# Kernel tuning notes

Hardware: AMD Instinct MI355X
Metric: run time of the kernel (lower is better)

The kernel has to match this reference:

```python
import jax, jax.numpy as jnp
import numpy as np

LM_TEMP = 2.0      # opts.lm_temp
LAMBDA_SH = 20.0   # lambda_sh passed in ot_loss
EPS = 1e-8


def sinkhorn(M, a, b, lam, num_iter_max=1000, stop_thr=0.005):
    """Faithful port of sinkhorn_pytorch. M:[S,V], a:[S,B], b:[V,B]."""
    K = jnp.exp(-M * lam)          # [S,V]
    KM = K * M
    u0 = jnp.ones_like(a) / a.shape[0]
    v0 = jnp.zeros_like(b)

    def cond(state):
        cpt, u, v, err = state
        return (cpt < num_iter_max) & (err > stop_thr)

    def body(state):
        cpt, u, v, err = state
        u = a / (K @ (b / (u.T @ K).T))   # fused fixed-point step
        cpt = cpt + 1
        do_check = ((cpt % 20) == 1) | (cpt == num_iter_max)

        def check(uve):
            u, v, _ = uve
            v = b / (K.T @ u)
            u = a / (K @ v)
            bb = v * (K.T @ u)
            err = jnp.max(jnp.sum(jnp.abs(bb - b), axis=0))  # inf-norm over batch
            return u, v, err

        u, v, err = jax.lax.cond(do_check, check, lambda t: t, (u, v, err))
        return cpt, u, v, err

    state0 = (jnp.asarray(0, jnp.int32), u0, v0, jnp.asarray(1.0, M.dtype))
    _, u, v, _ = jax.lax.while_loop(cond, body, state0)
    return jnp.sum(u * (KM @ v), axis=0)   # [B] sinkhorn divergences


def setup_inputs() -> dict:
    key = jax.random.key(0)
    ks = jax.random.split(key, 6)
    B, H, V, NV, MAX_SLOTS = 512, 1024, 28996, 3000, 33
    inputs = jax.random.normal(ks[0], (B, 2 * H), jnp.float32)
    outputs = jax.random.normal(ks[1], (B, 512), jnp.float32)
    W_lm = jax.random.normal(ks[2], (V, H), jnp.float32) * 0.02   # lm head (no bias)
    W_lin = jax.random.normal(ks[3], (MAX_SLOTS, 512), jnp.float32) * 0.05
    b_lin = jnp.zeros((MAX_SLOTS,), jnp.float32)
    topics = jax.random.normal(ks[4], (MAX_SLOTS - 1, H), jnp.float32) * 0.01
    verbs = jax.random.randint(ks[5], (NV,), 0, V)
    return {"inputs": inputs, "outputs": outputs, "W_lm": W_lm,
            "W_lin": W_lin, "b_lin": b_lin, "topics": topics,
            "verbs": verbs, "nslots": 33}


def reference(inputs, outputs, W_lm, W_lin, b_lin, topics, verbs, nslots):
    H = W_lm.shape[1]
    # gather verb rows of the lm head once: logits[:, verbs] == x @ W_lm[verbs].T
    W_v = W_lm[verbs]                               # [NV, H]
    Wt = W_v.T                                      # [H, NV]
    o11 = jax.nn.softmax((inputs[:, :H] @ Wt) / LM_TEMP, axis=-1)
    o12 = jax.nn.softmax((inputs[:, H:] @ Wt) / LM_TEMP, axis=-1)
    o1 = (o11 + o12) * 0.5
    o1 = o1 / jnp.sum(o1, axis=1, keepdims=True)    # [B, NV] vocab marginals
    o2 = jax.nn.softmax((outputs @ W_lin.T + b_lin)[:, 1:nslots], axis=-1)  # [B, S]
    # cosine-distance cost matrix between topics and verb embeddings
    tn = topics[:nslots - 1]
    tn = tn / (jnp.linalg.norm(tn, axis=1, keepdims=True) + EPS)
    vn = W_v / (jnp.linalg.norm(W_v, axis=1, keepdims=True) + EPS)
    M = 1.0 - tn @ vn.T                             # [S, NV]
    # single chunk of ot_loss (B <= 1024): mean sinkhorn divergence
    return jnp.mean(sinkhorn(M, o2.T, o1.T, LAMBDA_SH))
```

## Files before the change

kernel.cpp:

```cpp
#include <hip/hip_runtime.h>

#define NV 3000
#define HH 1024
#define BB 512

typedef __attribute__((ext_vector_type(8))) short short8;
typedef __attribute__((ext_vector_type(4))) float floatx4;

__device__ __forceinline__ float wave_sum(float x) {
#pragma unroll
  for (int off = 32; off; off >>= 1) x += __shfl_xor(x, off, 64);
  return x;
}
__device__ __forceinline__ unsigned bf16r(float x) {
  unsigned u = __float_as_uint(x);
  u += 0x7fffu + ((u >> 16) & 1u);
  return u >> 16;
}
__device__ __forceinline__ void gload16(const void* g, void* l) {
  __builtin_amdgcn_global_load_lds(
      (const __attribute__((address_space(1))) unsigned*)g,
      (__attribute__((address_space(3))) unsigned*)l, 16, 0, 0);
}

__global__ __launch_bounds__(256) void norms_wb_kernel(
    const float* __restrict__ W_lm, const float* __restrict__ topics,
    const int* __restrict__ verbs, float* __restrict__ vninv,
    float* __restrict__ tninv, unsigned short* __restrict__ Wb) {
  int r = blockIdx.x, t = threadIdx.x;
  bool isW = r < 3072;
  int j = isW ? (r < NV ? r : NV - 1) : 0;
  const float* src = isW ? (W_lm + (size_t)verbs[j] * HH)
                         : (topics + (size_t)(r - 3072) * HH);
  float4 v = *(const float4*)(src + t * 4);
  if (isW) {
    *(uint2*)(Wb + (size_t)r * HH + t * 4) =
        make_uint2(bf16r(v.x) | (bf16r(v.y) << 16),
                   bf16r(v.z) | (bf16r(v.w) << 16));
  }
  float ss = v.x * v.x + v.y * v.y + v.z * v.z + v.w * v.w;
  ss = wave_sum(ss);
  __shared__ float sq[4];
  if ((t & 63) == 0) sq[t >> 6] = ss;
  __syncthreads();
  if (t == 0) {
    float inv = 1.0f / (sqrtf(sq[0] + sq[1] + sq[2] + sq[3]) + 1e-8f);
    if (isW) { if (r < NV) vninv[r] = inv; }
    else tninv[r - 3072] = inv;
  }
}

__global__ __launch_bounds__(256) void xb_kernel(
    const float* __restrict__ inputs, unsigned short* __restrict__ Xb) {
  int idx = blockIdx.x * 256 + threadIdx.x;
  int r = idx >> 7, c8 = (idx & 127) << 3;
  const float* src = (r < 512) ? (inputs + (size_t)r * 2048 + c8)
                               : (inputs + (size_t)(r - 512) * 2048 + 1024 + c8);
  float4 x0 = ((const float4*)src)[0];
  float4 x1 = ((const float4*)src)[1];
  uint4 o;
  o.x = bf16r(x0.x) | (bf16r(x0.y) << 16);
  o.y = bf16r(x0.z) | (bf16r(x0.w) << 16);
  o.z = bf16r(x1.x) | (bf16r(x1.y) << 16);
  o.w = bf16r(x1.z) | (bf16r(x1.w) << 16);
  *(uint4*)(Xb + (size_t)r * HH + c8) = o;
}

__global__ __launch_bounds__(256) void topt_kernel(
    const float* __restrict__ topics, const float* __restrict__ tninv,
    float* __restrict__ topT) {
  int idx = blockIdx.x * 256 + threadIdx.x;
  int k = idx >> 5, s = idx & 31;
  topT[idx] = topics[(size_t)s * HH + k] * tninv[s];
}

__global__ __launch_bounds__(64) void a_kernel(
    const float* __restrict__ outputs, const float* __restrict__ W_lin,
    const float* __restrict__ b_lin, float* __restrict__ aT) {
  int r = blockIdx.x, t = threadIdx.x;
  __shared__ float orow[512];
  __shared__ float lg[33];
  __shared__ float ms[2];
  *(float4*)(orow + t * 8)     = *(const float4*)(outputs + (size_t)r * 512 + t * 8);
  *(float4*)(orow + t * 8 + 4) = *(const float4*)(outputs + (size_t)r * 512 + t * 8 + 4);
  __syncthreads();
  if (t < 33) {
    float acc = b_lin[t];
    for (int k = 0; k < 512; ++k) acc = fmaf(orow[k], W_lin[(size_t)t * 512 + k], acc);
    lg[t] = acc;
  }
  __syncthreads();
  if (t == 0) {
    float m = lg[1];
    for (int i = 2; i < 33; ++i) m = fmaxf(m, lg[i]);
    float ssum = 0.0f;
    for (int i = 1; i < 33; ++i) ssum += __expf(lg[i] - m);
    ms[0] = m; ms[1] = ssum;
  }
  __syncthreads();
  if (t >= 1 && t < 33) aT[(size_t)r * 32 + t - 1] = __expf(lg[t] - ms[0]) / ms[1];
}

__global__ __launch_bounds__(256) void gemm_mfma(
    const unsigned short* __restrict__ Xb, const unsigned short* __restrict__ Wb,
    float* __restrict__ L) {
  __shared__ unsigned short As[128 * 32], Bs[128 * 32];
  int t = threadIdx.x;
  int wave = t >> 6, ln = t & 63;
  int bn = blockIdx.x, bm = blockIdx.y;
  int wm = (wave >> 1) * 64, wn = (wave & 1) * 64;
  const unsigned short* ga = Xb + (size_t)(bm * 128 + (t >> 2)) * HH + (t & 3) * 8;
  const unsigned short* gb = Wb + (size_t)(bn * 128 + (t >> 2)) * HH + (t & 3) * 8;
  int lq = ln >> 4, lm = ln & 15;
  floatx4 acc[4][4];
#pragma unroll
  for (int i = 0; i < 4; ++i)
#pragma unroll
    for (int j = 0; j < 4; ++j) acc[i][j] = (floatx4)0.0f;

  for (int k0 = 0; k0 < HH; k0 += 32) {
    __syncthreads();
    gload16(ga + k0, As + t * 8);
    gload16(ga + (size_t)64 * HH + k0, As + 2048 + t * 8);
    gload16(gb + k0, Bs + t * 8);
    gload16(gb + (size_t)64 * HH + k0, Bs + 2048 + t * 8);
    __syncthreads();
    short8 af[4], bfr[4];
#pragma unroll
    for (int i = 0; i < 4; ++i)
      af[i] = *(const short8*)(As + (wm + i * 16 + lm) * 32 + lq * 8);
#pragma unroll
    for (int j = 0; j < 4; ++j)
      bfr[j] = *(const short8*)(Bs + (wn + j * 16 + lm) * 32 + lq * 8);
#pragma unroll
    for (int i = 0; i < 4; ++i)
#pragma unroll
      for (int j = 0; j < 4; ++j)
        acc[i][j] = __builtin_amdgcn_mfma_f32_16x16x32_bf16(af[i], bfr[j], acc[i][j], 0, 0, 0);
  }
  int row0 = bm * 128 + wm + lq * 4;
  int col0 = bn * 128 + wn + lm;
#pragma unroll
  for (int j = 0; j < 4; ++j) {
    int col = col0 + j * 16;
    if (col < NV) {
#pragma unroll
      for (int i = 0; i < 4; ++i) {
#pragma unroll
        for (int r = 0; r < 4; ++r)
          L[(size_t)(row0 + i * 16 + r) * NV + col] = acc[i][j][r] * 0.5f;
      }
    }
  }
}

__global__ __launch_bounds__(256) void softmax_kernel(
    float* __restrict__ L1, const float* __restrict__ L2) {
  int r = blockIdx.x, t = threadIdx.x, w = t >> 6, ln = t & 63;
  float* row1 = L1 + (size_t)r * NV;
  const float* row2 = L2 + (size_t)r * NV;
  __shared__ float rd[2][4];
  float s1 = 0.0f, s2 = 0.0f;
  for (int v = t; v < NV; v += 256) { s1 += __expf(row1[v]); s2 += __expf(row2[v]); }
  s1 = wave_sum(s1); s2 = wave_sum(s2);
  if (ln == 0) { rd[0][w] = s1; rd[1][w] = s2; }
  __syncthreads();
  s1 = rd[0][0] + rd[0][1] + rd[0][2] + rd[0][3];
  s2 = rd[1][0] + rd[1][1] + rd[1][2] + rd[1][3];
  float i1 = 0.5f / s1, i2 = 0.5f / s2;
  float rs = 0.0f;
  for (int v = t; v < NV; v += 256) {
    float o = __expf(row1[v]) * i1 + __expf(row2[v]) * i2;
    row1[v] = o; rs += o;
  }
  rs = wave_sum(rs);
  __syncthreads();
  if (ln == 0) rd[0][w] = rs;
  __syncthreads();
  float rinv = 1.0f / (rd[0][0] + rd[0][1] + rd[0][2] + rd[0][3]);
  for (int v = t; v < NV; v += 256) row1[v] *= rinv;
}

__global__ __launch_bounds__(256) void mk_kernel(
    const float* __restrict__ W_lm, const int* __restrict__ verbs,
    const float* __restrict__ topT, const float* __restrict__ vninv,
    unsigned* __restrict__ Kb, float* __restrict__ KMt) {
  __shared__ float red[4][64][33];
  int t = threadIdx.x, ln = t & 63, w = t >> 6;
  int v = blockIdx.x * 64 + ln;
  int vc = v < NV ? v : NV - 1;
  int kb = __builtin_amdgcn_readfirstlane(w) << 8;
  const float* wrow = W_lm + (size_t)verbs[vc] * HH + kb;
  const float* tb = topT + (size_t)kb * 32;
  float acc[32];
#pragma unroll
  for (int s = 0; s < 32; ++s) acc[s] = 0.0f;
  for (int kk = 0; kk < 256; kk += 4) {
    float4 w4 = *(const float4*)(wrow + kk);
    const float* tr = tb + kk * 32;
    const float* pw = (const float*)&w4;
#pragma unroll
    for (int d = 0; d < 4; ++d)
#pragma unroll
      for (int s = 0; s < 32; ++s) acc[s] = fmaf(pw[d], tr[d * 32 + s], acc[s]);
  }
#pragma unroll
  for (int s = 0; s < 32; ++s) red[w][ln][s] = acc[s];
  __syncthreads();
  for (int idx = t; idx < 1024; idx += 256) {
    int l = idx >> 4, pr = idx & 15;
    int vo = blockIdx.x * 64 + l;
    if (vo < NV) {
      int s0 = pr * 2, s1 = s0 + 1;
      float vi = vninv[vo];
      float d0 = red[0][l][s0] + red[1][l][s0] + red[2][l][s0] + red[3][l][s0];
      float d1 = red[0][l][s1] + red[1][l][s1] + red[2][l][s1] + red[3][l][s1];
      float M0 = 1.0f - d0 * vi, M1 = 1.0f - d1 * vi;
      float K0 = __expf(-20.0f * M0), K1 = __expf(-20.0f * M1);
      *(float2*)(KMt + (size_t)vo * 32 + s0) = make_float2(K0 * M0, K1 * M1);
      Kb[(size_t)vo * 16 + pr] = bf16r(K0) | (bf16r(K1) << 16);
    }
  }
}

__device__ __forceinline__ void gridbar(unsigned* bar, unsigned target) {
  __syncthreads();
  if (threadIdx.x == 0) {
    __hip_atomic_fetch_add(bar, 1u, __ATOMIC_RELEASE, __HIP_MEMORY_SCOPE_AGENT);
    while (__hip_atomic_load(bar, __ATOMIC_ACQUIRE, __HIP_MEMORY_SCOPE_AGENT) < target) {
      __builtin_amdgcn_s_sleep(1);
    }
  }
  __syncthreads();
}

#define UNPK(q, o)                                          \
  kc[(o) + 0] = __uint_as_float((q).x << 16);               \
  kc[(o) + 1] = __uint_as_float((q).x & 0xffff0000u);       \
  kc[(o) + 2] = __uint_as_float((q).y << 16);               \
  kc[(o) + 3] = __uint_as_float((q).y & 0xffff0000u);       \
  kc[(o) + 4] = __uint_as_float((q).z << 16);               \
  kc[(o) + 5] = __uint_as_float((q).z & 0xffff0000u);       \
  kc[(o) + 6] = __uint_as_float((q).w << 16);               \
  kc[(o) + 7] = __uint_as_float((q).w & 0xffff0000u);

template <bool STORE_T>
__device__ __forceinline__ void kpass_ss(
    const uint4* __restrict__ Kb, const float* __restrict__ bsh0,
    const float* __restrict__ bsh1, const float* u0, const float* u1,
    float* z0, float* z1, float* vsh0, float* vsh1, int pid, int p) {
#pragma unroll 3
  for (int i = 0; i < 6; ++i) {
    int v = pid + (i << 9);
    if (i < 5 || v < NV) {
      const uint4* kq = Kb + ((size_t)v << 2) + (p << 1);
      uint4 q0 = kq[0], q1 = kq[1];
      float kc[16];
      UNPK(q0, 0) UNPK(q1, 8)
      float w0 = 0.0f, w1 = 0.0f;
#pragma unroll
      for (int s = 0; s < 16; ++s) { w0 = fmaf(kc[s], u0[s], w0); w1 = fmaf(kc[s], u1[s], w1); }
      w0 += __shfl_xor(w0, 1, 64);
      w1 += __shfl_xor(w1, 1, 64);
      float t0 = bsh0[v] * __builtin_amdgcn_rcpf(w0);
      float t1 = bsh1[v] * __builtin_amdgcn_rcpf(w1);
      if (STORE_T && !p) { vsh0[v] = t0; vsh1[v] = t1; }
#pragma unroll
      for (int s = 0; s < 16; ++s) { z0[s] = fmaf(kc[s], t0, z0[s]); z1[s] = fmaf(kc[s], t1, z1[s]); }
    }
  }
}

__device__ __forceinline__ void errpass_ss(
    const uint4* __restrict__ Kb, const float* __restrict__ bsh0,
    const float* __restrict__ bsh1, const float* u0, const float* u1,
    const float* vsh0, const float* vsh1, float& ep0, float& ep1,
    int pid, int p) {
#pragma unroll 3
  for (int i = 0; i < 6; ++i) {
    int v = pid + (i << 9);
    if (i < 5 || v < NV) {
      const uint4* kq = Kb + ((size_t)v << 2) + (p << 1);
      uint4 q0 = kq[0], q1 = kq[1];
      float kc[16];
      UNPK(q0, 0) UNPK(q1, 8)
      float w0 = 0.0f, w1 = 0.0f;
#pragma unroll
      for (int s = 0; s < 16; ++s) { w0 = fmaf(kc[s], u0[s], w0); w1 = fmaf(kc[s], u1[s], w1); }
      w0 += __shfl_xor(w0, 1, 64);
      w1 += __shfl_xor(w1, 1, 64);
      if (!p) {
        ep0 += fabsf(vsh0[v] * w0 - bsh0[v]);
        ep1 += fabsf(vsh1[v] * w1 - bsh1[v]);
      }
    }
  }
}

__device__ __forceinline__ float waveRS16(float* z, int ln) {
  int cnt = 16;
#pragma unroll
  for (int d = 2; d <= 16; d <<= 1) {
    int half = cnt >> 1;
    bool hi = (ln & d) != 0;
#pragma unroll
    for (int k = 0; k < 8; ++k) {
      if (k < half) {
        float a = z[k], b = z[half + k];
        z[k] = hi ? b : a;
        z[half + k] = hi ? a : b;
      }
    }
#pragma unroll
    for (int k = 0; k < 8; ++k)
      if (k < half) z[k] += __shfl_xor(z[half + k], d, 64);
    cnt = half;
  }
  return z[0] + __shfl_xor(z[0], 32, 64);
}

__global__ __launch_bounds__(1024) void sinkhorn_kernel(
    const uint4* __restrict__ Kb, const float* __restrict__ KMt,
    const float* __restrict__ bT, const float* __restrict__ aT,
    unsigned* __restrict__ slots, float* __restrict__ outp) {
  const int t = threadIdx.x;
  const int w = t >> 6, ln = t & 63;
  const int p = t & 1, pid = t >> 1;
  const int col0 = blockIdx.x << 1;
  const float* b0r = bT + (size_t)col0 * NV;
  const float* b1r = b0r + NV;
  float* accres = (float*)(slots + 64);
  unsigned* bar = slots + 65;

  __shared__ float zred[2][16][32];
  __shared__ float ush[2][32];
  __shared__ float sredA[16], sredB[16];
  __shared__ unsigned ebits;
  __shared__ float vsh0[3072], vsh1[3072];
  __shared__ float bsh0[3072], bsh1[3072];
  float* ushf = &ush[0][0];

  const int sl = ((ln & 1) << 4) | ((ln & 2) << 2) | (ln & 4) |
                 ((ln & 8) >> 2) | ((ln & 16) >> 4);

  for (int idx = t; idx < NV; idx += 1024) { bsh0[idx] = b0r[idx]; bsh1[idx] = b1r[idx]; }
  float areg = (t < 64) ? aT[(size_t)col0 * 32 + t] : 0.0f;

  float u0[16], u1[16];
#pragma unroll
  for (int s = 0; s < 16; ++s) { u0[s] = 1.0f / 32.0f; u1[s] = 1.0f / 32.0f; }
  if (t < 64) ushf[t] = 1.0f / 32.0f;
  __syncthreads();
  float err = 1.0f;
  int cpt = 0, chk = 0;
  unsigned barcnt = 0;

  while (cpt < 1000 && err > 0.005f) {
    float z0[16], z1[16];
#pragma unroll
    for (int s = 0; s < 16; ++s) { z0[s] = 0.0f; z1[s] = 0.0f; }
    kpass_ss<false>(Kb, bsh0, bsh1, u0, u1, z0, z1, vsh0, vsh1, pid, p);
    float r0 = waveRS16(z0, ln), r1 = waveRS16(z1, ln);
    __syncthreads();
    if (ln < 32) { zred[0][w][sl] = r0; zred[1][w][sl] = r1; }
    __syncthreads();
    if (t < 64) {
      int c = t >> 5, s = t & 31;
      float zz = 0.0f;
#pragma unroll
      for (int k = 0; k < 16; ++k) zz += zred[c][k][s];
      ushf[t] = areg * __builtin_amdgcn_rcpf(zz);
    }
    __syncthreads();
#pragma unroll
    for (int q = 0; q < 4; ++q) {
      *(float4*)(u0 + q * 4) = *(float4*)(&ush[0][(p << 4) + q * 4]);
      *(float4*)(u1 + q * 4) = *(float4*)(&ush[1][(p << 4) + q * 4]);
    }
    ++cpt;

    if (cpt % 20 == 1 || cpt == 1000) {
#pragma unroll
      for (int s = 0; s < 16; ++s) { z0[s] = 0.0f; z1[s] = 0.0f; }
      kpass_ss<true>(Kb, bsh0, bsh1, u0, u1, z0, z1, vsh0, vsh1, pid, p);
      r0 = waveRS16(z0, ln); r1 = waveRS16(z1, ln);
      __syncthreads();
      if (ln < 32) { zred[0][w][sl] = r0; zred[1][w][sl] = r1; }
      __syncthreads();
      if (t < 64) {
        int c = t >> 5, s = t & 31;
        float zz = 0.0f;
#pragma unroll
        for (int k = 0; k < 16; ++k) zz += zred[c][k][s];
        ushf[t] = areg * __builtin_amdgcn_rcpf(zz);
      }
      __syncthreads();
#pragma unroll
      for (int q = 0; q < 4; ++q) {
        *(float4*)(u0 + q * 4) = *(float4*)(&ush[0][(p << 4) + q * 4]);
        *(float4*)(u1 + q * 4) = *(float4*)(&ush[1][(p << 4) + q * 4]);
      }
      float ep0 = 0.0f, ep1 = 0.0f;
      errpass_ss(Kb, bsh0, bsh1, u0, u1, vsh0, vsh1, ep0, ep1, pid, p);
      ep0 = wave_sum(ep0); ep1 = wave_sum(ep1);
      if (ln == 0) { sredA[w] = ep0; sredB[w] = ep1; }
      __syncthreads();
      if (t == 0) {
        float e0 = 0.0f, e1 = 0.0f;
#pragma unroll
        for (int k = 0; k < 16; ++k) { e0 += sredA[k]; e1 += sredB[k]; }
        atomicMax(slots + chk, __float_as_uint(fmaxf(e0, e1)));
      }
      ++barcnt;
      gridbar(bar, barcnt * 256u);
      if (t == 0) ebits = __hip_atomic_load(slots + chk, __ATOMIC_RELAXED, __HIP_MEMORY_SCOPE_AGENT);
      __syncthreads();
      err = __uint_as_float(ebits);
      ++chk;
    }
  }

  float y0[16], y1[16];
#pragma unroll
  for (int s = 0; s < 16; ++s) { y0[s] = 0.0f; y1[s] = 0.0f; }
#pragma unroll 3
  for (int i = 0; i < 6; ++i) {
    int v = pid + (i << 9);
    if (i < 5 || v < NV) {
      const float4* kp = (const float4*)(KMt + (size_t)v * 32 + (p << 4));
      float kc[16];
#pragma unroll
      for (int q = 0; q < 4; ++q) *(float4*)(kc + q * 4) = kp[q];
      float x0 = vsh0[v], x1 = vsh1[v];
#pragma unroll
      for (int s = 0; s < 16; ++s) { y0[s] = fmaf(kc[s], x0, y0[s]); y1[s] = fmaf(kc[s], x1, y1[s]); }
    }
  }
  float r0 = waveRS16(y0, ln), r1 = waveRS16(y1, ln);
  __syncthreads();
  if (ln < 32) { zred[0][w][sl] = r0; zred[1][w][sl] = r1; }
  __syncthreads();
  if (t < 64) {
    int c = t >> 5, s = t & 31;
    float ys = 0.0f;
#pragma unroll
    for (int k = 0; k < 16; ++k) ys += zred[c][k][s];
    float pp = ys * ushf[t];
#pragma unroll
    for (int off = 1; off <= 16; off <<= 1) pp += __shfl_xor(pp, off, 64);
    float other = __shfl_xor(pp, 32, 64);
    if (t == 0) atomicAdd(accres, pp + other);
  }
  ++barcnt;
  gridbar(bar, barcnt * 256u);
  if (blockIdx.x == 0 && t == 0) {
    unsigned ab = __hip_atomic_load((unsigned*)accres, __ATOMIC_RELAXED, __HIP_MEMORY_SCOPE_AGENT);
    outp[0] = __uint_as_float(ab) / 512.0f;
  }
}

extern "C" void kernel_launch(void* const* d_in, const int* in_sizes, int n_in,
                              void* d_out, int out_size, void* d_ws, size_t ws_size,
                              hipStream_t stream) {
  (void)in_sizes; (void)n_in; (void)out_size; (void)ws_size;
  const float* inputs  = (const float*)d_in[0];
  const float* outputs = (const float*)d_in[1];
  const float* W_lm    = (const float*)d_in[2];
  const float* W_lin   = (const float*)d_in[3];
  const float* b_lin   = (const float*)d_in[4];
  const float* topics  = (const float*)d_in[5];
  const int*   verbs   = (const int*)d_in[6];
  float* out = (float*)d_out;

  char* ws = (char*)d_ws;
  float*    L     = (float*)(ws);
  float*    L1    = L;
  float*    L2    = (float*)(ws + 6144000);
  float*    aT    = (float*)(ws + 12288000);
  unsigned* Kb    = (unsigned*)(ws + 12353536);
  float*    KMt   = (float*)(ws + 12545536);
  float*    topT  = (float*)(ws + 12929536);
  float*    vninv = (float*)(ws + 13060608);
  float*    tninv = (float*)(ws + 13072640);
  unsigned* slots = (unsigned*)(ws + 13072768);
  unsigned short* Xb = (unsigned short*)(ws + 13073280);
  unsigned short* Wb = (unsigned short*)(ws + 15170432);

  hipMemsetAsync((void*)slots, 0, 512, stream);

  norms_wb_kernel<<<3104, 256, 0, stream>>>(W_lm, topics, verbs, vninv, tninv, Wb);
  xb_kernel<<<512, 256, 0, stream>>>(inputs, Xb);
  topt_kernel<<<128, 256, 0, stream>>>(topics, tninv, topT);
  a_kernel<<<BB, 64, 0, stream>>>(outputs, W_lin, b_lin, aT);
  gemm_mfma<<<dim3(24, 8), 256, 0, stream>>>(Xb, Wb, L);
  softmax_kernel<<<BB, 256, 0, stream>>>(L1, L2);
  mk_kernel<<<47, 256, 0, stream>>>(W_lm, verbs, topT, vninv, Kb, KMt);
  sinkhorn_kernel<<<256, 1024, 0, stream>>>((const uint4*)Kb, KMt, L1, aT, slots, out);
}
```

Measured before the change: 412.7 us.

## Store Sinkhorn kernel matrix in per-column scaled FP8 and fold error pass into next iteration

The Sinkhorn K matrix is now stored as FP8 with a per-verb scale factor (KM is multiplied by the same factor), halving the bytes read on every iteration. The separate error-check pass is removed: the residual is instead accumulated during the following regular iteration's K·u product, which removes one full pass over K per check. Smaller changes come along: softmax caches exponentials in LDS instead of recomputing them, the a_kernel dot product is vectorised, and the gload helper is inlined. FP8 quantisation of K risks accuracy loss, and deferring the error check by one iteration may change when the loop stops.

```diff
diff --git a/kernel.cpp b/kernel.cpp
--- a/kernel.cpp
+++ b/kernel.cpp
@@ -6,6 +6,7 @@
 
 typedef __attribute__((ext_vector_type(8))) short short8;
 typedef __attribute__((ext_vector_type(4))) float floatx4;
+typedef __attribute__((ext_vector_type(2))) float floatx2;
 
 __device__ __forceinline__ float wave_sum(float x) {
 #pragma unroll
@@ -17,10 +18,36 @@
   u += 0x7fffu + ((u >> 16) & 1u);
   return u >> 16;
 }
-__device__ __forceinline__ void gload16(const void* g, void* l) {
-  __builtin_amdgcn_global_load_lds(
-      (const __attribute__((address_space(1))) unsigned*)g,
-      (__attribute__((address_space(3))) unsigned*)l, 16, 0, 0);
+
+__device__ __forceinline__ unsigned pk4_fp8(float a, float b, float c, float d) {
+#if __has_builtin(__builtin_amdgcn_cvt_pk_fp8_f32)
+  int r = __builtin_amdgcn_cvt_pk_fp8_f32(a, b, 0, false);
+  r = __builtin_amdgcn_cvt_pk_fp8_f32(c, d, r, true);
+  return (unsigned)r;
+#else
+  float v4[4] = {a, b, c, d};
+  unsigned out = 0;
+#pragma unroll
+  for (int i = 0; i < 4; ++i) {
+    unsigned bb = __float_as_uint(v4[i]);
+    bb += 0x7ffffu + ((bb >> 20) & 1u);
+    int e8 = (int)(bb >> 23) - 120;
+    unsigned byte = (e8 <= 0) ? 0u : (((unsigned)e8 << 3) | ((bb >> 20) & 7u));
+    out |= byte << (8 * i);
+  }
+  return out;
+#endif
+}
+__device__ __forceinline__ void unpk4(unsigned q, float* kc) {
+#if __has_builtin(__builtin_amdgcn_cvt_pk_f32_fp8)
+  floatx2 lo = __builtin_amdgcn_cvt_pk_f32_fp8((int)q, false);
+  floatx2 hi = __builtin_amdgcn_cvt_pk_f32_fp8((int)q, true);
+  kc[0] = lo[0]; kc[1] = lo[1]; kc[2] = hi[0]; kc[3] = hi[1];
+#else
+#pragma unroll
+  for (int i = 0; i < 4; ++i)
+    kc[i] = __uint_as_float((((q >> (8 * i)) & 0x7fu) << 20) + 0x3C000000u) - 0.0078125f;
+#endif
 }
 
 __global__ __launch_bounds__(256) void norms_wb_kernel(
@@ -85,9 +112,14 @@
   *(float4*)(orow + t * 8 + 4) = *(const float4*)(outputs + (size_t)r * 512 + t * 8 + 4);
   __syncthreads();
   if (t < 33) {
-    float acc = b_lin[t];
-    for (int k = 0; k < 512; ++k) acc = fmaf(orow[k], W_lin[(size_t)t * 512 + k], acc);
-    lg[t] = acc;
+    float4 a4 = make_float4(0.f, 0.f, 0.f, 0.f);
+    for (int k = 0; k < 512; k += 4) {
+      float4 o = *(const float4*)(orow + k);
+      float4 wl = *(const float4*)(W_lin + (size_t)t * 512 + k);
+      a4.x = fmaf(o.x, wl.x, a4.x); a4.y = fmaf(o.y, wl.y, a4.y);
+      a4.z = fmaf(o.z, wl.z, a4.z); a4.w = fmaf(o.w, wl.w, a4.w);
+    }
+    lg[t] = a4.x + a4.y + a4.z + a4.w + b_lin[t];
   }
   __syncthreads();
   if (t == 0) {
@@ -120,10 +152,18 @@
 
   for (int k0 = 0; k0 < HH; k0 += 32) {
     __syncthreads();
-    gload16(ga + k0, As + t * 8);
-    gload16(ga + (size_t)64 * HH + k0, As + 2048 + t * 8);
-    gload16(gb + k0, Bs + t * 8);
-    gload16(gb + (size_t)64 * HH + k0, Bs + 2048 + t * 8);
+    __builtin_amdgcn_global_load_lds(
+        (const __attribute__((address_space(1))) unsigned*)(ga + k0),
+        (__attribute__((address_space(3))) unsigned*)(As + t * 8), 16, 0, 0);
+    __builtin_amdgcn_global_load_lds(
+        (const __attribute__((address_space(1))) unsigned*)(ga + (size_t)64 * HH + k0),
+        (__attribute__((address_space(3))) unsigned*)(As + 2048 + t * 8), 16, 0, 0);
+    __builtin_amdgcn_global_load_lds(
+        (const __attribute__((address_space(1))) unsigned*)(gb + k0),
+        (__attribute__((address_space(3))) unsigned*)(Bs + t * 8), 16, 0, 0);
+    __builtin_amdgcn_global_load_lds(
+        (const __attribute__((address_space(1))) unsigned*)(gb + (size_t)64 * HH + k0),
+        (__attribute__((address_space(3))) unsigned*)(Bs + 2048 + t * 8), 16, 0, 0);
     __syncthreads();
     short8 af[4], bfr[4];
 #pragma unroll
@@ -159,9 +199,13 @@
   int r = blockIdx.x, t = threadIdx.x, w = t >> 6, ln = t & 63;
   float* row1 = L1 + (size_t)r * NV;
   const float* row2 = L2 + (size_t)r * NV;
+  __shared__ float e1[NV], e2[NV];
   __shared__ float rd[2][4];
   float s1 = 0.0f, s2 = 0.0f;
-  for (int v = t; v < NV; v += 256) { s1 += __expf(row1[v]); s2 += __expf(row2[v]); }
+  for (int v = t; v < NV; v += 256) {
+    float a = __expf(row1[v]), b = __expf(row2[v]);
+    e1[v] = a; e2[v] = b; s1 += a; s2 += b;
+  }
   s1 = wave_sum(s1); s2 = wave_sum(s2);
   if (ln == 0) { rd[0][w] = s1; rd[1][w] = s2; }
   __syncthreads();
@@ -170,22 +214,23 @@
   float i1 = 0.5f / s1, i2 = 0.5f / s2;
   float rs = 0.0f;
   for (int v = t; v < NV; v += 256) {
-    float o = __expf(row1[v]) * i1 + __expf(row2[v]) * i2;
-    row1[v] = o; rs += o;
+    float o = e1[v] * i1 + e2[v] * i2;
+    e1[v] = o; rs += o;
   }
   rs = wave_sum(rs);
   __syncthreads();
   if (ln == 0) rd[0][w] = rs;
   __syncthreads();
   float rinv = 1.0f / (rd[0][0] + rd[0][1] + rd[0][2] + rd[0][3]);
-  for (int v = t; v < NV; v += 256) row1[v] *= rinv;
+  for (int v = t; v < NV; v += 256) row1[v] = e1[v] * rinv;
 }
 
 __global__ __launch_bounds__(256) void mk_kernel(
     const float* __restrict__ W_lm, const int* __restrict__ verbs,
     const float* __restrict__ topT, const float* __restrict__ vninv,
-    unsigned* __restrict__ Kb, float* __restrict__ KMt) {
+    unsigned* __restrict__ Kb8, float* __restrict__ KMt) {
   __shared__ float red[4][64][33];
+  __shared__ float kv[64][33], km[64][33];
   int t = threadIdx.x, ln = t & 63, w = t >> 6;
   int v = blockIdx.x * 64 + ln;
   int vc = v < NV ? v : NV - 1;
@@ -207,18 +252,32 @@
 #pragma unroll
   for (int s = 0; s < 32; ++s) red[w][ln][s] = acc[s];
   __syncthreads();
-  for (int idx = t; idx < 1024; idx += 256) {
-    int l = idx >> 4, pr = idx & 15;
+  for (int idx = t; idx < 2048; idx += 256) {
+    int l = idx >> 5, s = idx & 31;
     int vo = blockIdx.x * 64 + l;
+    float vi = vninv[vo < NV ? vo : NV - 1];
+    float d = red[0][l][s] + red[1][l][s] + red[2][l][s] + red[3][l][s];
+    float M = 1.0f - d * vi;
+    float K = __expf(-20.0f * M);
+    kv[l][s] = K; km[l][s] = K * M;
+  }
+  __syncthreads();
+  if (t < 64) {
+    int vo = blockIdx.x * 64 + t;
     if (vo < NV) {
-      int s0 = pr * 2, s1 = s0 + 1;
-      float vi = vninv[vo];
-      float d0 = red[0][l][s0] + red[1][l][s0] + red[2][l][s0] + red[3][l][s0];
-      float d1 = red[0][l][s1] + red[1][l][s1] + red[2][l][s1] + red[3][l][s1];
-      float M0 = 1.0f - d0 * vi, M1 = 1.0f - d1 * vi;
-      float K0 = __expf(-20.0f * M0), K1 = __expf(-20.0f * M1);
-      *(float2*)(KMt + (size_t)vo * 32 + s0) = make_float2(K0 * M0, K1 * M1);
-      Kb[(size_t)vo * 16 + pr] = bf16r(K0) | (bf16r(K1) << 16);
+      float mx = 0.0f;
+#pragma unroll
+      for (int s = 0; s < 32; ++s) mx = fmaxf(mx, kv[t][s]);
+      float c = 240.0f / mx;
+      unsigned pk[8];
+#pragma unroll
+      for (int q = 0; q < 8; ++q)
+        pk[q] = pk4_fp8(kv[t][4 * q] * c, kv[t][4 * q + 1] * c,
+                        kv[t][4 * q + 2] * c, kv[t][4 * q + 3] * c);
+      *(uint4*)(Kb8 + (size_t)vo * 8)     = make_uint4(pk[0], pk[1], pk[2], pk[3]);
+      *(uint4*)(Kb8 + (size_t)vo * 8 + 4) = make_uint4(pk[4], pk[5], pk[6], pk[7]);
+#pragma unroll
+      for (int s = 0; s < 32; ++s) KMt[(size_t)vo * 32 + s] = km[t][s] * c;
     }
   }
 }
@@ -234,65 +293,34 @@
   __syncthreads();
 }
 
-#define UNPK(q, o)                                          \
-  kc[(o) + 0] = __uint_as_float((q).x << 16);               \
-  kc[(o) + 1] = __uint_as_float((q).x & 0xffff0000u);       \
-  kc[(o) + 2] = __uint_as_float((q).y << 16);               \
-  kc[(o) + 3] = __uint_as_float((q).y & 0xffff0000u);       \
-  kc[(o) + 4] = __uint_as_float((q).z << 16);               \
-  kc[(o) + 5] = __uint_as_float((q).z & 0xffff0000u);       \
-  kc[(o) + 6] = __uint_as_float((q).w << 16);               \
-  kc[(o) + 7] = __uint_as_float((q).w & 0xffff0000u);
-
-template <bool STORE_T>
+template <bool STORE_T, bool MEASURE>
 __device__ __forceinline__ void kpass_ss(
-    const uint4* __restrict__ Kb, const float* __restrict__ bsh0,
+    const uint4* __restrict__ Kb8, const float* __restrict__ bsh0,
     const float* __restrict__ bsh1, const float* u0, const float* u1,
-    float* z0, float* z1, float* vsh0, float* vsh1, int pid, int p) {
+    float* z0, float* z1, float* vsh0, float* vsh1,
+    float& ep0, float& ep1, int pid, int p) {
 #pragma unroll 3
   for (int i = 0; i < 6; ++i) {
     int v = pid + (i << 9);
     if (i < 5 || v < NV) {
-      const uint4* kq = Kb + ((size_t)v << 2) + (p << 1);
-      uint4 q0 = kq[0], q1 = kq[1];
+      uint4 q = Kb8[(size_t)v * 2 + p];
       float kc[16];
-      UNPK(q0, 0) UNPK(q1, 8)
+      unpk4(q.x, kc); unpk4(q.y, kc + 4); unpk4(q.z, kc + 8); unpk4(q.w, kc + 12);
       float w0 = 0.0f, w1 = 0.0f;
 #pragma unroll
       for (int s = 0; s < 16; ++s) { w0 = fmaf(kc[s], u0[s], w0); w1 = fmaf(kc[s], u1[s], w1); }
       w0 += __shfl_xor(w0, 1, 64);
       w1 += __shfl_xor(w1, 1, 64);
-      float t0 = bsh0[v] * __builtin_amdgcn_rcpf(w0);
-      float t1 = bsh1[v] * __builtin_amdgcn_rcpf(w1);
+      float b0v = bsh0[v], b1v = bsh1[v];
+      if (MEASURE && !p) {
+        ep0 += fabsf(vsh0[v] * w0 - b0v);
+        ep1 += fabsf(vsh1[v] * w1 - b1v);
+      }
+      float t0 = b0v * __builtin_amdgcn_rcpf(w0);
+      float t1 = b1v * __builtin_amdgcn_rcpf(w1);
       if (STORE_T && !p) { vsh0[v] = t0; vsh1[v] = t1; }
 #pragma unroll
       for (int s = 0; s < 16; ++s) { z0[s] = fmaf(kc[s], t0, z0[s]); z1[s] = fmaf(kc[s], t1, z1[s]); }
-    }
-  }
-}
-
-__device__ __forceinline__ void errpass_ss(
-    const uint4* __restrict__ Kb, const float* __restrict__ bsh0,
-    const float* __restrict__ bsh1, const float* u0, const float* u1,
-    const float* vsh0, const float* vsh1, float& ep0, float& ep1,
-    int pid, int p) {
-#pragma unroll 3
-  for (int i = 0; i < 6; ++i) {
-    int v = pid + (i << 9);
-    if (i < 5 || v < NV) {
-      const uint4* kq = Kb + ((size_t)v << 2) + (p << 1);
-      uint4 q0 = kq[0], q1 = kq[1];
-      float kc[16];
-      UNPK(q0, 0) UNPK(q1, 8)
-      float w0 = 0.0f, w1 = 0.0f;
-#pragma unroll
-      for (int s = 0; s < 16; ++s) { w0 = fmaf(kc[s], u0[s], w0); w1 = fmaf(kc[s], u1[s], w1); }
-      w0 += __shfl_xor(w0, 1, 64);
-      w1 += __shfl_xor(w1, 1, 64);
-      if (!p) {
-        ep0 += fabsf(vsh0[v] * w0 - bsh0[v]);
-        ep1 += fabsf(vsh1[v] * w1 - bsh1[v]);
-      }
     }
   }
 }
@@ -320,7 +348,7 @@
 }
 
 __global__ __launch_bounds__(1024) void sinkhorn_kernel(
-    const uint4* __restrict__ Kb, const float* __restrict__ KMt,
+    const uint4* __restrict__ Kb8, const float* __restrict__ KMt,
     const float* __restrict__ bT, const float* __restrict__ aT,
     unsigned* __restrict__ slots, float* __restrict__ outp) {
   const int t = threadIdx.x;
@@ -351,15 +379,19 @@
   for (int s = 0; s < 16; ++s) { u0[s] = 1.0f / 32.0f; u1[s] = 1.0f / 32.0f; }
   if (t < 64) ushf[t] = 1.0f / 32.0f;
   __syncthreads();
-  float err = 1.0f;
+  float err = 1.0f, ep0 = 0.0f, ep1 = 0.0f;
   int cpt = 0, chk = 0;
   unsigned barcnt = 0;
+  bool measuring = false;
 
   while (cpt < 1000 && err > 0.005f) {
     float z0[16], z1[16];
 #pragma unroll
     for (int s = 0; s < 16; ++s) { z0[s] = 0.0f; z1[s] = 0.0f; }
-    kpass_ss<false>(Kb, bsh0, bsh1, u0, u1, z0, z1, vsh0, vsh1, pid, p);
+    if (measuring)
+      kpass_ss<false, true>(Kb8, bsh0, bsh1, u0, u1, z0, z1, vsh0, vsh1, ep0, ep1, pid, p);
+    else
+      kpass_ss<false, false>(Kb8, bsh0, bsh1, u0, u1, z0, z1, vsh0, vsh1, ep0, ep1, pid, p);
     float r0 = waveRS16(z0, ln), r1 = waveRS16(z1, ln);
     __syncthreads();
     if (ln < 32) { zred[0][w][sl] = r0; zred[1][w][sl] = r1; }
@@ -379,29 +411,7 @@
     }
     ++cpt;
 
-    if (cpt % 20 == 1 || cpt == 1000) {
-#pragma unroll
-      for (int s = 0; s < 16; ++s) { z0[s] = 0.0f; z1[s] = 0.0f; }
-      kpass_ss<true>(Kb, bsh0, bsh1, u0, u1, z0, z1, vsh0, vsh1, pid, p);
-      r0 = waveRS16(z0, ln); r1 = waveRS16(z1, ln);
-      __syncthreads();
-      if (ln < 32) { zred[0][w][sl] = r0; zred[1][w][sl] = r1; }
-      __syncthreads();
-      if (t < 64) {
-        int c = t >> 5, s = t & 31;
-        float zz = 0.0f;
-#pragma unroll
-        for (int k = 0; k < 16; ++k) zz += zred[c][k][s];
-        ushf[t] = areg * __builtin_amdgcn_rcpf(zz);
-      }
-      __syncthreads();
-#pragma unroll
-      for (int q = 0; q < 4; ++q) {
-        *(float4*)(u0 + q * 4) = *(float4*)(&ush[0][(p << 4) + q * 4]);
-        *(float4*)(u1 + q * 4) = *(float4*)(&ush[1][(p << 4) + q * 4]);
-      }
-      float ep0 = 0.0f, ep1 = 0.0f;
-      errpass_ss(Kb, bsh0, bsh1, u0, u1, vsh0, vsh1, ep0, ep1, pid, p);
+    if (measuring) {
       ep0 = wave_sum(ep0); ep1 = wave_sum(ep1);
       if (ln == 0) { sredA[w] = ep0; sredB[w] = ep1; }
       __syncthreads();
@@ -417,6 +427,32 @@
       __syncthreads();
       err = __uint_as_float(ebits);
       ++chk;
+      ep0 = 0.0f; ep1 = 0.0f;
+      measuring = false;
+    }
+
+    if (err > 0.005f && cpt % 20 == 1) {
+#pragma unroll
+      for (int s = 0; s < 16; ++s) { z0[s] = 0.0f; z1[s] = 0.0f; }
+      kpass_ss<true, false>(Kb8, bsh0, bsh1, u0, u1, z0, z1, vsh0, vsh1, ep0, ep1, pid, p);
+      r0 = waveRS16(z0, ln); r1 = waveRS16(z1, ln);
+      __syncthreads();
+      if (ln < 32) { zred[0][w][sl] = r0; zred[1][w][sl] = r1; }
+      __syncthreads();
+      if (t < 64) {
+        int c = t >> 5, s = t & 31;
+        float zz = 0.0f;
+#pragma unroll
+        for (int k = 0; k < 16; ++k) zz += zred[c][k][s];
+        ushf[t] = areg * __builtin_amdgcn_rcpf(zz);
+      }
+      __syncthreads();
+#pragma unroll
+      for (int q = 0; q < 4; ++q) {
+        *(float4*)(u0 + q * 4) = *(float4*)(&ush[0][(p << 4) + q * 4]);
+        *(float4*)(u1 + q * 4) = *(float4*)(&ush[1][(p << 4) + q * 4]);
+      }
+      measuring = true;
     }
   }
 
@@ -477,14 +513,14 @@
   float*    L1    = L;
   float*    L2    = (float*)(ws + 6144000);
   float*    aT    = (float*)(ws + 12288000);
-  unsigned* Kb    = (unsigned*)(ws + 12353536);
-  float*    KMt   = (float*)(ws + 12545536);
-  float*    topT  = (float*)(ws + 12929536);
-  float*    vninv = (float*)(ws + 13060608);
-  float*    tninv = (float*)(ws + 13072640);
-  unsigned* slots = (unsigned*)(ws + 13072768);
-  unsigned short* Xb = (unsigned short*)(ws + 13073280);
-  unsigned short* Wb = (unsigned short*)(ws + 15170432);
+  unsigned* Kb8   = (unsigned*)(ws + 12353536);
+  float*    KMt   = (float*)(ws + 12449536);
+  float*    topT  = (float*)(ws + 12833536);
+  float*    vninv = (float*)(ws + 12964608);
+  float*    tninv = (float*)(ws + 12976640);
+  unsigned* slots = (unsigned*)(ws + 12976768);
+  unsigned short* Xb = (unsigned short*)(ws + 12977280);
+  unsigned short* Wb = (unsigned short*)(ws + 15074432);
 
   hipMemsetAsync((void*)slots, 0, 512, stream);
 
@@ -494,6 +530,6 @@
   a_kernel<<<BB, 64, 0, stream>>>(outputs, W_lin, b_lin, aT);
   gemm_mfma<<<dim3(24, 8), 256, 0, stream>>>(Xb, Wb, L);
   softmax_kernel<<<BB, 256, 0, stream>>>(L1, L2);
-  mk_kernel<<<47, 256, 0, stream>>>(W_lm, verbs, topT, vninv, Kb, KMt);
-  sinkhorn_kernel<<<256, 1024, 0, stream>>>((const uint4*)Kb, KMt, L1, aT, slots, out);
-}
+  mk_kernel<<<47, 256, 0, stream>>>(W_lm, verbs, topT, vninv, Kb8, KMt);
+  sinkhorn_kernel<<<256, 1024, 0, stream>>>((const uint4*)Kb8, KMt, L1, aT, slots, out);
+}
```

Result: slower. 424.7 us (+2.9%).
